# Performance work log

Hardware: AMD Instinct MI355X
Metric: run time of the kernel (lower is better)

Reference implementation:

```python
import jax, jax.numpy as jnp
import numpy as np

N_NODES = 50000
N_EDGES = 1600000
D_IN = 128
D_OUT = 32
N_HEADS = 4


def setup_inputs() -> dict:
    key = jax.random.key(0)
    k1, k2, k3, k4 = jax.random.split(key, 4)
    x = jax.random.normal(k1, (N_NODES, D_IN), dtype=jnp.float32)
    edge_index = jax.random.randint(k2, (2, N_EDGES), 0, N_NODES, dtype=jnp.int64)
    W = jax.random.normal(k3, (N_HEADS, D_IN, D_OUT), dtype=jnp.float32) * 0.01
    a = jax.random.normal(k4, (N_HEADS, 2 * D_OUT), dtype=jnp.float32) * 0.01
    return {"x": x, "edge_index": edge_index, "W": W, "a": a}


def reference(x, edge_index, W, a):
    N = x.shape[0]
    K, d_in, d_out = W.shape
    # Per-head projected node features: [N, K, d_out]
    Wh = jnp.einsum('ni,kio->nko', x, W)
    src, tgt = edge_index[0], edge_index[1]
    # cat([Wh[src], Wh[tgt]]) . a  ==  Wh[src].a[:, :d] + Wh[tgt].a[:, d:]
    s_src = jnp.einsum('nkd,kd->nk', Wh, a[:, :d_out])  # [N, K]
    s_tgt = jnp.einsum('nkd,kd->nk', Wh, a[:, d_out:])  # [N, K]
    e = s_src[src] + s_tgt[tgt]                          # [E, K]
    e = jnp.where(e > 0, e, 0.2 * e)                     # LeakyReLU(0.2)
    # Segment-softmax over incoming edges of each target node
    e_max = jax.ops.segment_max(e, tgt, num_segments=N)  # [N, K], -inf for empty
    e_max = jnp.where(jnp.isfinite(e_max), e_max, 0.0)
    e_exp = jnp.exp(e - e_max[tgt])                      # [E, K]
    e_sum = jax.ops.segment_sum(e_exp, tgt, num_segments=N)  # [N, K]
    alpha = e_exp / (e_sum[tgt] + 1e-10)                 # [E, K]
    # Weighted scatter-add aggregation: [N, K, d_out]
    weighted = alpha[:, :, None] * Wh[src]
    out = jax.ops.segment_sum(weighted, tgt, num_segments=N)
    out = out.reshape(N, K * d_out)
    return jnp.where(out > 0, out, jnp.expm1(out))       # ELU
```

## Files before the change

kernel.cpp:

```cpp
#include <hip/hip_runtime.h>
#include <math.h>

#define N_HEADS 4
#define D_IN    128
#define D_OUT   32
#define TN      64
#define XPAD    132
#define BSH     6
#define BNODES  64
#define EPT     16
#define CAP     2560
#define BT      512
#define NW      8
#define QNODES  16
#define ORDQ    2688

static __device__ __forceinline__ unsigned short f2bf(float f) {
    unsigned u = __float_as_uint(f);
    u += 0x7fffu + ((u >> 16) & 1u);
    return (unsigned short)(u >> 16);
}

__global__ __launch_bounds__(256) void front_kernel(
    const float* __restrict__ x,
    const float* __restrict__ W,
    const float* __restrict__ a,
    const int*  __restrict__ ei,
    int*  __restrict__ cursor,
    unsigned int* __restrict__ bbuf,
    unsigned int* __restrict__ Whu,
    float* __restrict__ s_src,
    float* __restrict__ s_tgt,
    int N, int E, int nProj, int nb) {

    __shared__ float xs[TN][XPAD];
    const int t = threadIdx.x;

    if (blockIdx.x >= nProj) {
        int* cnt = (int*)xs;
        for (int i = t; i < nb; i += 256) cnt[i] = 0;
        __syncthreads();

        const int e0 = (blockIdx.x - nProj) * (256 * EPT);
        int src[EPT], tgt[EPT];
        #pragma unroll
        for (int i = 0; i < EPT; ++i) {
            int e = e0 + i * 256 + t;
            if (e < E) {
                src[i] = ei[e];
                tgt[i] = ei[E + e];
                atomicAdd(&cnt[tgt[i] >> BSH], 1);
            } else {
                src[i] = -1; tgt[i] = 0;
            }
        }
        __syncthreads();
        for (int b = t; b < nb; b += 256)
            if (cnt[b]) cnt[b] = atomicAdd(&cursor[b], cnt[b]);
        __syncthreads();
        #pragma unroll
        for (int i = 0; i < EPT; ++i) {
            if (src[i] >= 0) {
                int b = tgt[i] >> BSH;
                int pos = atomicAdd(&cnt[b], 1);
                if (pos < CAP)
                    bbuf[(size_t)b * CAP + pos] =
                        ((unsigned)(tgt[i] & (BNODES - 1)) << 16) | (unsigned)src[i];
            }
        }
        return;
    }

    const int n0 = blockIdx.x * TN;
    {
        const int r  = t >> 2;
        const int c0 = (t & 3) * 32;
        int nn = n0 + r; if (nn >= N) nn = N - 1;
        const float4* src = (const float4*)(x + (size_t)nn * D_IN + c0);
        #pragma unroll
        for (int j = 0; j < 8; ++j)
            *(float4*)&xs[r][c0 + j * 4] = src[j];
    }
    __syncthreads();

    const int fg = t & 15;
    const int ng = t >> 4;
    const int f0 = fg * 8;
    const int k  = f0 >> 5;
    const int o0 = f0 & 31;
    const float* Wf = W + k * (D_IN * D_OUT) + o0;

    float acc[4][8];
    #pragma unroll
    for (int nl = 0; nl < 4; ++nl)
        #pragma unroll
        for (int j = 0; j < 8; ++j) acc[nl][j] = 0.f;

    #pragma unroll 2
    for (int i = 0; i < D_IN; i += 4) {
        float4 wa[4], wb[4];
        #pragma unroll
        for (int ii = 0; ii < 4; ++ii) {
            wa[ii] = *(const float4*)(Wf + (i + ii) * D_OUT);
            wb[ii] = *(const float4*)(Wf + (i + ii) * D_OUT + 4);
        }
        #pragma unroll
        for (int nl = 0; nl < 4; ++nl) {
            const float4 xv = *(const float4*)&xs[ng * 4 + nl][i];
            const float xr[4] = {xv.x, xv.y, xv.z, xv.w};
            #pragma unroll
            for (int ii = 0; ii < 4; ++ii) {
                acc[nl][0] = fmaf(xr[ii], wa[ii].x, acc[nl][0]);
                acc[nl][1] = fmaf(xr[ii], wa[ii].y, acc[nl][1]);
                acc[nl][2] = fmaf(xr[ii], wa[ii].z, acc[nl][2]);
                acc[nl][3] = fmaf(xr[ii], wa[ii].w, acc[nl][3]);
                acc[nl][4] = fmaf(xr[ii], wb[ii].x, acc[nl][4]);
                acc[nl][5] = fmaf(xr[ii], wb[ii].y, acc[nl][5]);
                acc[nl][6] = fmaf(xr[ii], wb[ii].z, acc[nl][6]);
                acc[nl][7] = fmaf(xr[ii], wb[ii].w, acc[nl][7]);
            }
        }
    }

    const float4 as0 = *(const float4*)(a + k * (2 * D_OUT) + o0);
    const float4 as1 = *(const float4*)(a + k * (2 * D_OUT) + o0 + 4);
    const float4 at0 = *(const float4*)(a + k * (2 * D_OUT) + D_OUT + o0);
    const float4 at1 = *(const float4*)(a + k * (2 * D_OUT) + D_OUT + o0 + 4);

    #pragma unroll
    for (int nl = 0; nl < 4; ++nl) {
        const int n = n0 + ng * 4 + nl;
        if (n < N) {
            unsigned int p[4];
            #pragma unroll
            for (int j = 0; j < 4; ++j)
                p[j] = (unsigned)f2bf(acc[nl][2 * j]) |
                       ((unsigned)f2bf(acc[nl][2 * j + 1]) << 16);
            *(uint4*)&Whu[(size_t)n * 64 + fg * 4] = make_uint4(p[0], p[1], p[2], p[3]);

            float vs = acc[nl][0] * as0.x + acc[nl][1] * as0.y +
                       acc[nl][2] * as0.z + acc[nl][3] * as0.w +
                       acc[nl][4] * as1.x + acc[nl][5] * as1.y +
                       acc[nl][6] * as1.z + acc[nl][7] * as1.w;
            float vt = acc[nl][0] * at0.x + acc[nl][1] * at0.y +
                       acc[nl][2] * at0.z + acc[nl][3] * at0.w +
                       acc[nl][4] * at1.x + acc[nl][5] * at1.y +
                       acc[nl][6] * at1.z + acc[nl][7] * at1.w;
            vs += __shfl_xor(vs, 1, 64); vs += __shfl_xor(vs, 2, 64);
            vt += __shfl_xor(vt, 1, 64); vt += __shfl_xor(vt, 2, 64);
            if ((fg & 3) == 0) {
                s_src[n * N_HEADS + k] = vs;
                s_tgt[n * N_HEADS + k] = vt;
            }
        }
    }
}

__global__ __launch_bounds__(BT) void bagg_kernel(
    const unsigned int* __restrict__ bbuf,
    const int* __restrict__ cursor,
    const float* __restrict__ s_src,
    const float* __restrict__ s_tgt,
    const unsigned int* __restrict__ Whu,
    float* __restrict__ out, int N) {

    __shared__ unsigned stg[CAP];
    __shared__ __align__(16) unsigned short ord[ORDQ];
    __shared__ int hist[QNODES], cur[QNODES];
    __shared__ int begs[QNODES], ends[QNODES];
    __shared__ float evs[NW][64];

    int bid = blockIdx.x;
    const int nwg = gridDim.x;
    if ((nwg & 7) == 0) {
        const int cpx = nwg >> 3;
        bid = (blockIdx.x & 7) * cpx + (blockIdx.x >> 3);
    }
    const int b       = bid >> 2;
    const int quarter = bid & 3;
    const int tt  = threadIdx.x;
    const int wid = tt >> 6;
    const int t   = tt & 63;
    const int k   = t >> 4;
    const int i16 = t & 15;

    if (tt < QNODES) hist[tt] = 0;
    for (int i = tt; i < ORDQ / 2; i += BT) ((unsigned*)ord)[i] = 0;
    __syncthreads();

    int cnt = cursor[b]; if (cnt > CAP) cnt = CAP;
    const unsigned* bbp = bbuf + (size_t)b * CAP;
    for (int i = tt; i < cnt; i += BT) {
        unsigned v = bbp[i];
        stg[i] = v;
        unsigned ln = v >> 16;
        if ((int)(ln >> 4) == quarter) atomicAdd(&hist[ln & (QNODES - 1)], 1);
    }
    __syncthreads();

    if (tt < QNODES) {
        int v = hist[tt];
        int vp = (v + 7) & ~7;
        int incl = vp;
        #pragma unroll
        for (int off = 1; off < QNODES; off <<= 1) {
            int tv = __shfl_up(incl, off, 64);
            if (tt >= off) incl += tv;
        }
        int excl = incl - vp;
        cur[tt]  = excl;
        begs[tt] = excl;
        ends[tt] = excl + v;
    }
    __syncthreads();

    for (int i = tt; i < cnt; i += BT) {
        unsigned v = stg[i];
        unsigned ln = v >> 16;
        if ((int)(ln >> 4) == quarter) {
            int pos = atomicAdd(&cur[ln & (QNODES - 1)], 1);
            ord[pos] = (unsigned short)(v & 0xffffu);
        }
    }
    __syncthreads();

    #pragma unroll
    for (int r2 = 0; r2 < QNODES / NW; ++r2) {
        const int lnl = (wid << 1) + r2;
        const int n   = b * BNODES + (quarter << 4) + lnl;
        const int beg = begs[lnl];
        const int end = ends[lnl];
        const float stk = s_tgt[((size_t)n << 2) + k];

        float denp = 0.f, nx = 0.f, ny = 0.f;
        for (int j = beg; j < end; j += 16) {
            const uint4 da = *(const uint4*)&ord[j];
            const uint4 db = *(const uint4*)&ord[j + 8];
            const int own = j + i16;
            const unsigned svo = ord[own];
            const float ssv = s_src[((size_t)svo << 2) + k];
            float av = ssv + stk;
            av = fmaxf(av, 0.2f * av);
            const float evv = (own < end) ? __expf(av) : 0.f;
            denp += evv;
            evs[wid][t] = evv;

            int sv[16];
            sv[0]  = (int)(da.x & 0xffffu); sv[1]  = (int)(da.x >> 16);
            sv[2]  = (int)(da.y & 0xffffu); sv[3]  = (int)(da.y >> 16);
            sv[4]  = (int)(da.z & 0xffffu); sv[5]  = (int)(da.z >> 16);
            sv[6]  = (int)(da.w & 0xffffu); sv[7]  = (int)(da.w >> 16);
            sv[8]  = (int)(db.x & 0xffffu); sv[9]  = (int)(db.x >> 16);
            sv[10] = (int)(db.y & 0xffffu); sv[11] = (int)(db.y >> 16);
            sv[12] = (int)(db.z & 0xffffu); sv[13] = (int)(db.z >> 16);
            sv[14] = (int)(db.w & 0xffffu); sv[15] = (int)(db.w >> 16);

            unsigned w[16];
            #pragma unroll
            for (int q = 0; q < 16; ++q)
                w[q] = Whu[((unsigned)sv[q] << 6) + (unsigned)t];

            float e[16];
            *(float4*)&e[0]  = *(const float4*)&evs[wid][(k << 4) + 0];
            *(float4*)&e[4]  = *(const float4*)&evs[wid][(k << 4) + 4];
            *(float4*)&e[8]  = *(const float4*)&evs[wid][(k << 4) + 8];
            *(float4*)&e[12] = *(const float4*)&evs[wid][(k << 4) + 12];

            #pragma unroll
            for (int q = 0; q < 16; ++q) {
                nx = fmaf(e[q], __uint_as_float(w[q] << 16), nx);
                ny = fmaf(e[q], __uint_as_float(w[q] & 0xffff0000u), ny);
            }
        }

        denp += __shfl_xor(denp, 1, 64);
        denp += __shfl_xor(denp, 2, 64);
        denp += __shfl_xor(denp, 4, 64);
        denp += __shfl_xor(denp, 8, 64);

        if (n < N) {
            const float inv = 1.f / (denp + 1e-10f);
            float ox = nx * inv, oy = ny * inv;
            ox = ox > 0.f ? ox : expm1f(ox);
            oy = oy > 0.f ? oy : expm1f(oy);
            *(float2*)&out[((size_t)n << 7) + (t << 1)] = make_float2(ox, oy);
        }
    }
}

extern "C" void kernel_launch(void* const* d_in, const int* in_sizes, int n_in,
                              void* d_out, int out_size, void* d_ws, size_t ws_size,
                              hipStream_t stream) {
    const float* x  = (const float*)d_in[0];
    const int*   ei = (const int*)d_in[1];
    const float* W  = (const float*)d_in[2];
    const float* a  = (const float*)d_in[3];
    float* out = (float*)d_out;

    const int N = in_sizes[0] / D_IN;
    const int E = in_sizes[1] / 2;
    const int nb = (N + BNODES - 1) >> BSH;

    char* p = (char*)d_ws;
    auto align256 = [](size_t v) { return (v + 255) & ~(size_t)255; };
    unsigned int* Whu = (unsigned int*)p;      p += align256((size_t)N * 64 * 4);
    float* s_src    = (float*)p;               p += align256((size_t)N * N_HEADS * 4);
    float* s_tgt    = (float*)p;               p += align256((size_t)N * N_HEADS * 4);
    const size_t curBytes = align256((size_t)nb * 4);
    int*   cursor   = (int*)p;                 p += curBytes;
    unsigned int* bbuf = (unsigned int*)p;

    hipMemsetAsync(cursor, 0, curBytes, stream);

    const int nProj = (N + TN - 1) / TN;
    const int nBkt  = (E + 256 * EPT - 1) / (256 * EPT);
    front_kernel<<<nProj + nBkt, 256, 0, stream>>>(
        x, W, a, ei, cursor, bbuf, Whu, s_src, s_tgt, N, E, nProj, nb);

    bagg_kernel<<<nb * 4, BT, 0, stream>>>(
        bbuf, cursor, s_src, s_tgt, Whu, out, N);
}
```

Measured before the change: 113.1 us.

## Stage W chunks in LDS and gather 8-byte feature pairs per lane in aggregation

The projection kernel now loads W into shared memory in 16-row chunks instead of having every thread read it from global memory, and drops the padding on the x tile. The aggregation loop is restructured so each lane fetches a uint2 (four bf16 features) for half of the 16 edges, with the two wave halves splitting even and odd edges and combining through a cross-half shuffle. This halves the number of gather instructions and widens each access. In exchange it adds extra block barriers per chunk in the projection, possible LDS bank conflicts on the unpadded x tile, and shuffle reductions with half the lanes idle at the store.

Result: slower. 191.8 us (+69.6%).

```diff
diff --git a/kernel.cpp b/kernel.cpp
--- a/kernel.cpp
+++ b/kernel.cpp
@@ -5,7 +5,6 @@
 #define D_IN    128
 #define D_OUT   32
 #define TN      64
-#define XPAD    132
 #define BSH     6
 #define BNODES  64
 #define EPT     16
@@ -33,7 +32,8 @@
     float* __restrict__ s_tgt,
     int N, int E, int nProj, int nb) {
 
-    __shared__ float xs[TN][XPAD];
+    __shared__ float xs[TN][128];
+    __shared__ float Wl[16][128];
     const int t = threadIdx.x;
 
     if (blockIdx.x >= nProj) {
@@ -81,14 +81,16 @@
         for (int j = 0; j < 8; ++j)
             *(float4*)&xs[r][c0 + j * 4] = src[j];
     }
-    __syncthreads();
 
     const int fg = t & 15;
     const int ng = t >> 4;
     const int f0 = fg * 8;
     const int k  = f0 >> 5;
     const int o0 = f0 & 31;
-    const float* Wf = W + k * (D_IN * D_OUT) + o0;
+
+    const int srow = t >> 4;
+    const int sc0  = (t & 15) * 8;
+    const float* Wst = W + (sc0 >> 5) * (D_IN * D_OUT) + (sc0 & 31);
 
     float acc[4][8];
     #pragma unroll
@@ -96,28 +98,41 @@
         #pragma unroll
         for (int j = 0; j < 8; ++j) acc[nl][j] = 0.f;
 
-    #pragma unroll 2
-    for (int i = 0; i < D_IN; i += 4) {
-        float4 wa[4], wb[4];
-        #pragma unroll
-        for (int ii = 0; ii < 4; ++ii) {
-            wa[ii] = *(const float4*)(Wf + (i + ii) * D_OUT);
-            wb[ii] = *(const float4*)(Wf + (i + ii) * D_OUT + 4);
-        }
-        #pragma unroll
-        for (int nl = 0; nl < 4; ++nl) {
-            const float4 xv = *(const float4*)&xs[ng * 4 + nl][i];
-            const float xr[4] = {xv.x, xv.y, xv.z, xv.w};
+    for (int ch = 0; ch < 8; ++ch) {
+        __syncthreads();
+        {
+            const int i = ch * 16 + srow;
+            const float4 w0 = *(const float4*)(Wst + i * D_OUT);
+            const float4 w1 = *(const float4*)(Wst + i * D_OUT + 4);
+            *(float4*)&Wl[srow][sc0]     = w0;
+            *(float4*)&Wl[srow][sc0 + 4] = w1;
+        }
+        __syncthreads();
+
+        #pragma unroll 2
+        for (int i4 = 0; i4 < 4; ++i4) {
+            const int ib = i4 * 4;
+            float4 wa[4], wb[4];
             #pragma unroll
             for (int ii = 0; ii < 4; ++ii) {
-                acc[nl][0] = fmaf(xr[ii], wa[ii].x, acc[nl][0]);
-                acc[nl][1] = fmaf(xr[ii], wa[ii].y, acc[nl][1]);
-                acc[nl][2] = fmaf(xr[ii], wa[ii].z, acc[nl][2]);
-                acc[nl][3] = fmaf(xr[ii], wa[ii].w, acc[nl][3]);
-                acc[nl][4] = fmaf(xr[ii], wb[ii].x, acc[nl][4]);
-                acc[nl][5] = fmaf(xr[ii], wb[ii].y, acc[nl][5]);
-                acc[nl][6] = fmaf(xr[ii], wb[ii].z, acc[nl][6]);
-                acc[nl][7] = fmaf(xr[ii], wb[ii].w, acc[nl][7]);
+                wa[ii] = *(const float4*)&Wl[ib + ii][f0];
+                wb[ii] = *(const float4*)&Wl[ib + ii][f0 + 4];
+            }
+            #pragma unroll
+            for (int nl = 0; nl < 4; ++nl) {
+                const float4 xv = *(const float4*)&xs[ng * 4 + nl][ch * 16 + ib];
+                const float xr[4] = {xv.x, xv.y, xv.z, xv.w};
+                #pragma unroll
+                for (int ii = 0; ii < 4; ++ii) {
+                    acc[nl][0] = fmaf(xr[ii], wa[ii].x, acc[nl][0]);
+                    acc[nl][1] = fmaf(xr[ii], wa[ii].y, acc[nl][1]);
+                    acc[nl][2] = fmaf(xr[ii], wa[ii].z, acc[nl][2]);
+                    acc[nl][3] = fmaf(xr[ii], wa[ii].w, acc[nl][3]);
+                    acc[nl][4] = fmaf(xr[ii], wb[ii].x, acc[nl][4]);
+                    acc[nl][5] = fmaf(xr[ii], wb[ii].y, acc[nl][5]);
+                    acc[nl][6] = fmaf(xr[ii], wb[ii].z, acc[nl][6]);
+                    acc[nl][7] = fmaf(xr[ii], wb[ii].w, acc[nl][7]);
+                }
             }
         }
     }
@@ -183,6 +198,9 @@
     const int t   = tt & 63;
     const int k   = t >> 4;
     const int i16 = t & 15;
+    const int h   = t >> 5;
+    const int u   = t & 31;
+    const int hd  = u >> 3;
 
     if (tt < QNODES) hist[tt] = 0;
     for (int i = tt; i < ORDQ / 2; i += BT) ((unsigned*)ord)[i] = 0;
@@ -232,7 +250,7 @@
         const int end = ends[lnl];
         const float stk = s_tgt[((size_t)n << 2) + k];
 
-        float denp = 0.f, nx = 0.f, ny = 0.f;
+        float denp = 0.f, a0 = 0.f, a1 = 0.f, a2 = 0.f, a3 = 0.f;
         for (int j = beg; j < end; j += 16) {
             const uint4 da = *(const uint4*)&ord[j];
             const uint4 db = *(const uint4*)&ord[j + 8];
@@ -245,31 +263,28 @@
             denp += evv;
             evs[wid][t] = evv;
 
-            int sv[16];
-            sv[0]  = (int)(da.x & 0xffffu); sv[1]  = (int)(da.x >> 16);
-            sv[2]  = (int)(da.y & 0xffffu); sv[3]  = (int)(da.y >> 16);
-            sv[4]  = (int)(da.z & 0xffffu); sv[5]  = (int)(da.z >> 16);
-            sv[6]  = (int)(da.w & 0xffffu); sv[7]  = (int)(da.w >> 16);
-            sv[8]  = (int)(db.x & 0xffffu); sv[9]  = (int)(db.x >> 16);
-            sv[10] = (int)(db.y & 0xffffu); sv[11] = (int)(db.y >> 16);
-            sv[12] = (int)(db.z & 0xffffu); sv[13] = (int)(db.z >> 16);
-            sv[14] = (int)(db.w & 0xffffu); sv[15] = (int)(db.w >> 16);
-
-            unsigned w[16];
-            #pragma unroll
-            for (int q = 0; q < 16; ++q)
-                w[q] = Whu[((unsigned)sv[q] << 6) + (unsigned)t];
+            const unsigned wd[8] = {da.x, da.y, da.z, da.w,
+                                    db.x, db.y, db.z, db.w};
+            uint2 g[8];
+            #pragma unroll
+            for (int q = 0; q < 8; ++q) {
+                const unsigned sv = h ? (wd[q] >> 16) : (wd[q] & 0xffffu);
+                g[q] = *(const uint2*)&Whu[(sv << 6) + (u << 1)];
+            }
 
             float e[16];
-            *(float4*)&e[0]  = *(const float4*)&evs[wid][(k << 4) + 0];
-            *(float4*)&e[4]  = *(const float4*)&evs[wid][(k << 4) + 4];
-            *(float4*)&e[8]  = *(const float4*)&evs[wid][(k << 4) + 8];
-            *(float4*)&e[12] = *(const float4*)&evs[wid][(k << 4) + 12];
-
-            #pragma unroll
-            for (int q = 0; q < 16; ++q) {
-                nx = fmaf(e[q], __uint_as_float(w[q] << 16), nx);
-                ny = fmaf(e[q], __uint_as_float(w[q] & 0xffff0000u), ny);
+            *(float4*)&e[0]  = *(const float4*)&evs[wid][(hd << 4) + 0];
+            *(float4*)&e[4]  = *(const float4*)&evs[wid][(hd << 4) + 4];
+            *(float4*)&e[8]  = *(const float4*)&evs[wid][(hd << 4) + 8];
+            *(float4*)&e[12] = *(const float4*)&evs[wid][(hd << 4) + 12];
+
+            #pragma unroll
+            for (int q = 0; q < 8; ++q) {
+                const float ee = e[2 * q + h];
+                a0 = fmaf(ee, __uint_as_float(g[q].x << 16),         a0);
+                a1 = fmaf(ee, __uint_as_float(g[q].x & 0xffff0000u), a1);
+                a2 = fmaf(ee, __uint_as_float(g[q].y << 16),         a2);
+                a3 = fmaf(ee, __uint_as_float(g[q].y & 0xffff0000u), a3);
             }
         }
 
@@ -277,13 +292,22 @@
         denp += __shfl_xor(denp, 2, 64);
         denp += __shfl_xor(denp, 4, 64);
         denp += __shfl_xor(denp, 8, 64);
-
-        if (n < N) {
-            const float inv = 1.f / (denp + 1e-10f);
-            float ox = nx * inv, oy = ny * inv;
-            ox = ox > 0.f ? ox : expm1f(ox);
-            oy = oy > 0.f ? oy : expm1f(oy);
-            *(float2*)&out[((size_t)n << 7) + (t << 1)] = make_float2(ox, oy);
+        const float dh = __shfl(denp, hd << 4, 64);
+
+        a0 += __shfl_xor(a0, 32, 64);
+        a1 += __shfl_xor(a1, 32, 64);
+        a2 += __shfl_xor(a2, 32, 64);
+        a3 += __shfl_xor(a3, 32, 64);
+
+        if (n < N && h == 0) {
+            const float inv = 1.f / (dh + 1e-10f);
+            float4 o;
+            o.x = a0 * inv; o.y = a1 * inv; o.z = a2 * inv; o.w = a3 * inv;
+            o.x = o.x > 0.f ? o.x : expm1f(o.x);
+            o.y = o.y > 0.f ? o.y : expm1f(o.y);
+            o.z = o.z > 0.f ? o.z : expm1f(o.z);
+            o.w = o.w > 0.f ? o.w : expm1f(o.w);
+            *(float4*)&out[((size_t)n << 7) + (u << 2)] = o;
         }
     }
 }
```
